# Kernel tuning notes

Measured on AMD Instinct MI355X. Metric: run time of the kernel, lower is better.

## Reference

```python
import jax, jax.numpy as jnp
import numpy as np

N_NODES = 100000
N_EDGES = 1600000
D_FEAT = 64
EPS = 1e-07


def setup_inputs() -> dict:
    key = jax.random.key(0)
    k1, k2, k3 = jax.random.split(key, 3)
    x = jax.random.normal(k1, (N_NODES, D_FEAT), dtype=jnp.float32)
    beta = jnp.ones((1,), dtype=jnp.float32)
    edge_row = jnp.sort(jax.random.randint(k2, (N_EDGES,), 0, N_NODES, dtype=jnp.int64))
    edge_col = jax.random.randint(k3, (N_EDGES,), 0, N_NODES, dtype=jnp.int64)
    return {"x": x, "beta": beta, "edge_row": edge_row, "edge_col": edge_col}


def reference(x, beta, edge_row, edge_col):
    # Gather endpoint features: [E, d]
    A = x[edge_row]
    B = x[edge_col]
    # Cosine similarity per edge, scaled by beta: [E]
    inner = jnp.sum(A * B, axis=1)
    norms = jnp.linalg.norm(A, axis=1) * jnp.linalg.norm(B, axis=1)
    sim = beta[0] * (inner / (norms + EPS))
    # Sparse row-wise softmax (tf.sparse.softmax): stable segment softmax over edges grouped by row
    row_max = jax.ops.segment_max(sim, edge_row, num_segments=N_NODES)
    e = jnp.exp(sim - row_max[edge_row])
    row_sum = jax.ops.segment_sum(e, edge_row, num_segments=N_NODES)
    p = e / row_sum[edge_row]  # [E]
    # SPMM: out[i] = sum_{(i,j) in E} p_ij * x[j]
    out = jax.ops.segment_sum(p[:, None] * B, edge_row, num_segments=N_NODES)
    return out
```

## Files before the change

### kernel.cpp

```cpp
#include <hip/hip_runtime.h>
#include <math.h>

#define D_FEAT 64

__global__ __launch_bounds__(256)
void agnn_rnorm(const float* __restrict__ x, float* __restrict__ rn, int n_nodes) {
    int t = blockIdx.x * blockDim.x + threadIdx.x;
    int node = t >> 4;
    if (node >= n_nodes) return;
    int l4 = t & 15;
    float4 v = ((const float4*)x)[node * 16 + l4];
    float ss = v.x * v.x + v.y * v.y + v.z * v.z + v.w * v.w;
    #pragma unroll
    for (int off = 1; off < 16; off <<= 1)
        ss += __shfl_xor(ss, off, 64);
    if (l4 == 0) rn[node] = ss > 0.f ? rsqrtf(ss) : 0.f;
}

__global__ __launch_bounds__(256)
void agnn_rowptr(const int* __restrict__ edge_row, int* __restrict__ row_ptr,
                 int n_nodes, int n_edges) {
    int e = blockIdx.x * blockDim.x + threadIdx.x;
    if (e >= n_edges) return;
    int r1 = edge_row[e];
    int r0 = (e == 0) ? -1 : edge_row[e - 1];
    for (int r = r0 + 1; r <= r1; ++r) row_ptr[r] = e;
    if (e == n_edges - 1) {
        for (int r = r1 + 1; r <= n_nodes; ++r) row_ptr[r] = n_edges;
    }
}

__global__ __launch_bounds__(256)
void agnn_fused(const float* __restrict__ x,
                const float* __restrict__ beta_p,
                const int* __restrict__ edge_col,
                const int* __restrict__ row_ptr,
                const float* __restrict__ rn,
                float* __restrict__ out, int n_nodes) {
    int node = (blockIdx.x * blockDim.x + threadIdx.x) >> 6;
    if (node >= n_nodes) return;
    int lane = threadIdx.x & 63;
    int g  = lane >> 4;
    int l4 = lane & 15;

    const float4* x4 = (const float4*)x;
    float4 xi  = x4[node * 16 + l4];
    float beta = beta_p[0];
    float brni = beta * rn[node];
    float shift = fabsf(beta);

    int es = row_ptr[node];
    int deg = row_ptr[node + 1] - es;

    float s = 0.f;
    float4 acc = {0.f, 0.f, 0.f, 0.f};

    for (int base = 0; base < deg; base += 8) {
        int ei0 = base + g;
        int ei1 = base + 4 + g;
        bool v0 = ei0 < deg;
        bool v1 = ei1 < deg;
        int ea = es + (v0 ? ei0 : 0);
        int eb = es + (v1 ? ei1 : 0);
        int c0 = edge_col[ea];
        int c1 = edge_col[eb];
        float4 a = x4[c0 * 16 + l4];
        float4 b = x4[c1 * 16 + l4];
        float rn0 = rn[c0];
        float rn1 = rn[c1];

        float d0 = a.x * xi.x + a.y * xi.y + a.z * xi.z + a.w * xi.w;
        float d1 = b.x * xi.x + b.y * xi.y + b.z * xi.z + b.w * xi.w;
        #pragma unroll
        for (int off = 1; off < 16; off <<= 1) {
            d0 += __shfl_xor(d0, off, 64);
            d1 += __shfl_xor(d1, off, 64);
        }

        float w0 = v0 ? __expf(brni * d0 * rn0 - shift) : 0.f;
        float w1 = v1 ? __expf(brni * d1 * rn1 - shift) : 0.f;
        s += w0 + w1;
        acc.x += w0 * a.x + w1 * b.x;
        acc.y += w0 * a.y + w1 * b.y;
        acc.z += w0 * a.z + w1 * b.z;
        acc.w += w0 * a.w + w1 * b.w;
    }

    #pragma unroll
    for (int off = 16; off < 64; off <<= 1) {
        s     += __shfl_xor(s,     off, 64);
        acc.x += __shfl_xor(acc.x, off, 64);
        acc.y += __shfl_xor(acc.y, off, 64);
        acc.z += __shfl_xor(acc.z, off, 64);
        acc.w += __shfl_xor(acc.w, off, 64);
    }

    if (g == 0) {
        float inv = (deg > 0 && s > 0.f) ? 1.f / s : 0.f;
        float4 o = {acc.x * inv, acc.y * inv, acc.z * inv, acc.w * inv};
        ((float4*)out)[node * 16 + l4] = o;
    }
}

extern "C" void kernel_launch(void* const* d_in, const int* in_sizes, int n_in,
                              void* d_out, int out_size, void* d_ws, size_t ws_size,
                              hipStream_t stream) {
    const float* x        = (const float*)d_in[0];
    const float* beta     = (const float*)d_in[1];
    const int*   edge_row = (const int*)d_in[2];
    const int*   edge_col = (const int*)d_in[3];
    float* out = (float*)d_out;

    int n_nodes = in_sizes[0] / D_FEAT;
    int n_edges = in_sizes[2];

    float* rn = (float*)d_ws;
    size_t rn_bytes = ((size_t)n_nodes * sizeof(float) + 255) & ~(size_t)255;
    int* row_ptr = (int*)((char*)d_ws + rn_bytes);

    {
        long long threads = (long long)n_nodes * 16;
        int blocks = (int)((threads + 255) / 256);
        agnn_rnorm<<<blocks, 256, 0, stream>>>(x, rn, n_nodes);
    }
    {
        int blocks = (n_edges + 255) / 256;
        agnn_rowptr<<<blocks, 256, 0, stream>>>(edge_row, row_ptr, n_nodes, n_edges);
    }
    {
        int blocks = (n_nodes + 3) / 4;
        agnn_fused<<<blocks, 256, 0, stream>>>(x, beta, edge_col, row_ptr, rn,
                                               out, n_nodes);
    }
}
```

Measured before the change: 150.3 us.

## Gather neighbor features from a bf16 copy with 8-lane edge groups

```diff
diff --git a/kernel.cpp b/kernel.cpp
--- a/kernel.cpp
+++ b/kernel.cpp
@@ -2,9 +2,17 @@
 #include <math.h>
 
 #define D_FEAT 64
+typedef unsigned int u32;
+
+__device__ __forceinline__ unsigned short f2bf_rne(float f) {
+    u32 u = __float_as_uint(f);
+    u32 r = u + 0x7FFFu + ((u >> 16) & 1u);
+    return (unsigned short)(r >> 16);
+}
 
 __global__ __launch_bounds__(256)
-void agnn_rnorm(const float* __restrict__ x, float* __restrict__ rn, int n_nodes) {
+void agnn_prep(const float* __restrict__ x, float* __restrict__ rn,
+               ushort4* __restrict__ xh, int n_nodes) {
     int t = blockIdx.x * blockDim.x + threadIdx.x;
     int node = t >> 4;
     if (node >= n_nodes) return;
@@ -15,6 +23,10 @@
     for (int off = 1; off < 16; off <<= 1)
         ss += __shfl_xor(ss, off, 64);
     if (l4 == 0) rn[node] = ss > 0.f ? rsqrtf(ss) : 0.f;
+    ushort4 h;
+    h.x = f2bf_rne(v.x); h.y = f2bf_rne(v.y);
+    h.z = f2bf_rne(v.z); h.w = f2bf_rne(v.w);
+    xh[node * 16 + l4] = h;
 }
 
 __global__ __launch_bounds__(256)
@@ -36,69 +48,82 @@
                 const int* __restrict__ edge_col,
                 const int* __restrict__ row_ptr,
                 const float* __restrict__ rn,
+                const ushort4* __restrict__ xh,
                 float* __restrict__ out, int n_nodes) {
     int node = (blockIdx.x * blockDim.x + threadIdx.x) >> 6;
     if (node >= n_nodes) return;
     int lane = threadIdx.x & 63;
-    int g  = lane >> 4;
-    int l4 = lane & 15;
+    int g  = lane >> 3;
+    int l8 = lane & 7;
 
     const float4* x4 = (const float4*)x;
-    float4 xi  = x4[node * 16 + l4];
+    float4 xiLo = x4[node * 16 + 2 * l8];
+    float4 xiHi = x4[node * 16 + 2 * l8 + 1];
     float beta = beta_p[0];
     float brni = beta * rn[node];
     float shift = fabsf(beta);
 
-    int es = row_ptr[node];
+    int es  = row_ptr[node];
     int deg = row_ptr[node + 1] - es;
 
     float s = 0.f;
-    float4 acc = {0.f, 0.f, 0.f, 0.f};
+    float4 accLo = {0.f, 0.f, 0.f, 0.f};
+    float4 accHi = {0.f, 0.f, 0.f, 0.f};
+
+    const uint4* xh4 = (const uint4*)xh;
 
     for (int base = 0; base < deg; base += 8) {
-        int ei0 = base + g;
-        int ei1 = base + 4 + g;
-        bool v0 = ei0 < deg;
-        bool v1 = ei1 < deg;
-        int ea = es + (v0 ? ei0 : 0);
-        int eb = es + (v1 ? ei1 : 0);
-        int c0 = edge_col[ea];
-        int c1 = edge_col[eb];
-        float4 a = x4[c0 * 16 + l4];
-        float4 b = x4[c1 * 16 + l4];
-        float rn0 = rn[c0];
-        float rn1 = rn[c1];
-
-        float d0 = a.x * xi.x + a.y * xi.y + a.z * xi.z + a.w * xi.w;
-        float d1 = b.x * xi.x + b.y * xi.y + b.z * xi.z + b.w * xi.w;
+        int ei = base + g;
+        bool valid = ei < deg;
+        float4 aLo = {0.f, 0.f, 0.f, 0.f};
+        float4 aHi = {0.f, 0.f, 0.f, 0.f};
+        float rnc = 0.f;
+        if (valid) {
+            int c = edge_col[es + ei];
+            uint4 u = xh4[(size_t)c * 8 + l8];
+            rnc = rn[c];
+            aLo.x = __uint_as_float(u.x << 16);
+            aLo.y = __uint_as_float(u.x & 0xFFFF0000u);
+            aLo.z = __uint_as_float(u.y << 16);
+            aLo.w = __uint_as_float(u.y & 0xFFFF0000u);
+            aHi.x = __uint_as_float(u.z << 16);
+            aHi.y = __uint_as_float(u.z & 0xFFFF0000u);
+            aHi.z = __uint_as_float(u.w << 16);
+            aHi.w = __uint_as_float(u.w & 0xFFFF0000u);
+        }
+        float d = aLo.x * xiLo.x + aLo.y * xiLo.y + aLo.z * xiLo.z + aLo.w * xiLo.w
+                + aHi.x * xiHi.x + aHi.y * xiHi.y + aHi.z * xiHi.z + aHi.w * xiHi.w;
         #pragma unroll
-        for (int off = 1; off < 16; off <<= 1) {
-            d0 += __shfl_xor(d0, off, 64);
-            d1 += __shfl_xor(d1, off, 64);
-        }
-
-        float w0 = v0 ? __expf(brni * d0 * rn0 - shift) : 0.f;
-        float w1 = v1 ? __expf(brni * d1 * rn1 - shift) : 0.f;
-        s += w0 + w1;
-        acc.x += w0 * a.x + w1 * b.x;
-        acc.y += w0 * a.y + w1 * b.y;
-        acc.z += w0 * a.z + w1 * b.z;
-        acc.w += w0 * a.w + w1 * b.w;
+        for (int off = 1; off < 8; off <<= 1)
+            d += __shfl_xor(d, off, 64);
+        float w = valid ? __expf(brni * d * rnc - shift) : 0.f;
+        s += w;
+        accLo.x += w * aLo.x; accLo.y += w * aLo.y;
+        accLo.z += w * aLo.z; accLo.w += w * aLo.w;
+        accHi.x += w * aHi.x; accHi.y += w * aHi.y;
+        accHi.z += w * aHi.z; accHi.w += w * aHi.w;
     }
 
     #pragma unroll
-    for (int off = 16; off < 64; off <<= 1) {
-        s     += __shfl_xor(s,     off, 64);
-        acc.x += __shfl_xor(acc.x, off, 64);
-        acc.y += __shfl_xor(acc.y, off, 64);
-        acc.z += __shfl_xor(acc.z, off, 64);
-        acc.w += __shfl_xor(acc.w, off, 64);
+    for (int off = 8; off < 64; off <<= 1) {
+        s       += __shfl_xor(s,       off, 64);
+        accLo.x += __shfl_xor(accLo.x, off, 64);
+        accLo.y += __shfl_xor(accLo.y, off, 64);
+        accLo.z += __shfl_xor(accLo.z, off, 64);
+        accLo.w += __shfl_xor(accLo.w, off, 64);
+        accHi.x += __shfl_xor(accHi.x, off, 64);
+        accHi.y += __shfl_xor(accHi.y, off, 64);
+        accHi.z += __shfl_xor(accHi.z, off, 64);
+        accHi.w += __shfl_xor(accHi.w, off, 64);
     }
 
     if (g == 0) {
         float inv = (deg > 0 && s > 0.f) ? 1.f / s : 0.f;
-        float4 o = {acc.x * inv, acc.y * inv, acc.z * inv, acc.w * inv};
-        ((float4*)out)[node * 16 + l4] = o;
+        float4 oLo = {accLo.x * inv, accLo.y * inv, accLo.z * inv, accLo.w * inv};
+        float4 oHi = {accHi.x * inv, accHi.y * inv, accHi.z * inv, accHi.w * inv};
+        float4* o4 = (float4*)out;
+        o4[node * 16 + 2 * l8]     = oLo;
+        o4[node * 16 + 2 * l8 + 1] = oHi;
     }
 }
 
@@ -114,14 +139,17 @@
     int n_nodes = in_sizes[0] / D_FEAT;
     int n_edges = in_sizes[2];
 
-    float* rn = (float*)d_ws;
-    size_t rn_bytes = ((size_t)n_nodes * sizeof(float) + 255) & ~(size_t)255;
-    int* row_ptr = (int*)((char*)d_ws + rn_bytes);
+    char* ws = (char*)d_ws;
+    float* rn = (float*)ws;
+    size_t off0 = ((size_t)n_nodes * sizeof(float) + 255) & ~(size_t)255;
+    int* row_ptr = (int*)(ws + off0);
+    size_t off1 = off0 + (((size_t)(n_nodes + 1) * sizeof(int) + 255) & ~(size_t)255);
+    ushort4* xh = (ushort4*)(ws + off1);
 
     {
         long long threads = (long long)n_nodes * 16;
         int blocks = (int)((threads + 255) / 256);
-        agnn_rnorm<<<blocks, 256, 0, stream>>>(x, rn, n_nodes);
+        agnn_prep<<<blocks, 256, 0, stream>>>(x, rn, xh, n_nodes);
     }
     {
         int blocks = (n_edges + 255) / 256;
@@ -130,6 +158,6 @@
     {
         int blocks = (n_nodes + 3) / 4;
         agnn_fused<<<blocks, 256, 0, stream>>>(x, beta, edge_col, row_ptr, rn,
-                                               out, n_nodes);
+                                               xh, out, n_nodes);
     }
 }
```

Result: faster. 144.5 us (-3.9%).

## Gather neighbor features in fp16 with dot2 and merge prep kernels

Applied to the files above, without the earlier changes.

```diff
diff --git a/kernel.cpp b/kernel.cpp
--- a/kernel.cpp
+++ b/kernel.cpp
@@ -2,31 +2,52 @@
 #include <math.h>
 
 #define D_FEAT 64
+typedef _Float16 h2 __attribute__((ext_vector_type(2)));
 
-__global__ __launch_bounds__(256)
-void agnn_rnorm(const float* __restrict__ x, float* __restrict__ rn, int n_nodes) {
-    int t = blockIdx.x * blockDim.x + threadIdx.x;
-    int node = t >> 4;
-    if (node >= n_nodes) return;
-    int l4 = t & 15;
-    float4 v = ((const float4*)x)[node * 16 + l4];
-    float ss = v.x * v.x + v.y * v.y + v.z * v.z + v.w * v.w;
-    #pragma unroll
-    for (int off = 1; off < 16; off <<= 1)
-        ss += __shfl_xor(ss, off, 64);
-    if (l4 == 0) rn[node] = ss > 0.f ? rsqrtf(ss) : 0.f;
+__device__ __forceinline__ float dot2(unsigned int a, h2 b, float c) {
+    h2 av; __builtin_memcpy(&av, &a, 4);
+#if __has_builtin(__builtin_amdgcn_fdot2)
+    return __builtin_amdgcn_fdot2(av, b, c, false);
+#else
+    return c + (float)av[0] * (float)b[0] + (float)av[1] * (float)b[1];
+#endif
+}
+
+__device__ __forceinline__ h2 bits2h2(unsigned int a) {
+    h2 av; __builtin_memcpy(&av, &a, 4);
+    return av;
 }
 
 __global__ __launch_bounds__(256)
-void agnn_rowptr(const int* __restrict__ edge_row, int* __restrict__ row_ptr,
-                 int n_nodes, int n_edges) {
-    int e = blockIdx.x * blockDim.x + threadIdx.x;
-    if (e >= n_edges) return;
-    int r1 = edge_row[e];
-    int r0 = (e == 0) ? -1 : edge_row[e - 1];
-    for (int r = r0 + 1; r <= r1; ++r) row_ptr[r] = e;
-    if (e == n_edges - 1) {
-        for (int r = r1 + 1; r <= n_nodes; ++r) row_ptr[r] = n_edges;
+void agnn_prep(const float* __restrict__ x, float* __restrict__ rn,
+               uint2* __restrict__ xh, const int* __restrict__ edge_row,
+               int* __restrict__ row_ptr, int n_nodes, int n_edges, int nb_prep) {
+    if ((int)blockIdx.x < nb_prep) {
+        int t = blockIdx.x * blockDim.x + threadIdx.x;
+        int node = t >> 4;
+        if (node >= n_nodes) return;
+        int l4 = t & 15;
+        float4 v = ((const float4*)x)[node * 16 + l4];
+        float ss = v.x * v.x + v.y * v.y + v.z * v.z + v.w * v.w;
+        #pragma unroll
+        for (int off = 1; off < 16; off <<= 1)
+            ss += __shfl_xor(ss, off, 64);
+        if (l4 == 0) rn[node] = ss > 0.f ? rsqrtf(ss) : 0.f;
+        h2 h0 = {( _Float16)v.x, (_Float16)v.y};
+        h2 h1 = {( _Float16)v.z, (_Float16)v.w};
+        uint2 u;
+        __builtin_memcpy(&u.x, &h0, 4);
+        __builtin_memcpy(&u.y, &h1, 4);
+        xh[node * 16 + l4] = u;
+    } else {
+        int e = (blockIdx.x - nb_prep) * blockDim.x + threadIdx.x;
+        if (e >= n_edges) return;
+        int r1 = edge_row[e];
+        int r0 = (e == 0) ? -1 : edge_row[e - 1];
+        for (int r = r0 + 1; r <= r1; ++r) row_ptr[r] = e;
+        if (e == n_edges - 1) {
+            for (int r = r1 + 1; r <= n_nodes; ++r) row_ptr[r] = n_edges;
+        }
     }
 }
 
@@ -36,43 +57,61 @@
                 const int* __restrict__ edge_col,
                 const int* __restrict__ row_ptr,
                 const float* __restrict__ rn,
+                const uint4* __restrict__ xh4,
                 float* __restrict__ out, int n_nodes) {
     int node = (blockIdx.x * blockDim.x + threadIdx.x) >> 6;
     if (node >= n_nodes) return;
     int lane = threadIdx.x & 63;
-    int g  = lane >> 4;
-    int l4 = lane & 15;
+    int g  = lane >> 3;
+    int l8 = lane & 7;
 
     const float4* x4 = (const float4*)x;
-    float4 xi  = x4[node * 16 + l4];
+    float4 xiLo = x4[node * 16 + 2 * l8];
+    float4 xiHi = x4[node * 16 + 2 * l8 + 1];
+    h2 xi0 = {( _Float16)xiLo.x, (_Float16)xiLo.y};
+    h2 xi1 = {( _Float16)xiLo.z, (_Float16)xiLo.w};
+    h2 xi2 = {( _Float16)xiHi.x, (_Float16)xiHi.y};
+    h2 xi3 = {( _Float16)xiHi.z, (_Float16)xiHi.w};
+
     float beta = beta_p[0];
     float brni = beta * rn[node];
     float shift = fabsf(beta);
 
-    int es = row_ptr[node];
+    int es  = row_ptr[node];
     int deg = row_ptr[node + 1] - es;
 
     float s = 0.f;
-    float4 acc = {0.f, 0.f, 0.f, 0.f};
+    h2 acc0 = {0, 0}, acc1 = {0, 0}, acc2 = {0, 0}, acc3 = {0, 0};
 
-    for (int base = 0; base < deg; base += 8) {
+    for (int base = 0; base < deg; base += 16) {
         int ei0 = base + g;
-        int ei1 = base + 4 + g;
+        int ei1 = base + 8 + g;
         bool v0 = ei0 < deg;
         bool v1 = ei1 < deg;
-        int ea = es + (v0 ? ei0 : 0);
-        int eb = es + (v1 ? ei1 : 0);
-        int c0 = edge_col[ea];
-        int c1 = edge_col[eb];
-        float4 a = x4[c0 * 16 + l4];
-        float4 b = x4[c1 * 16 + l4];
-        float rn0 = rn[c0];
-        float rn1 = rn[c1];
+        uint4 u0 = {0, 0, 0, 0};
+        uint4 u1 = {0, 0, 0, 0};
+        float rn0 = 0.f, rn1 = 0.f;
+        if (v0) {
+            int c = edge_col[es + ei0];
+            u0 = xh4[(size_t)c * 8 + l8];
+            rn0 = rn[c];
+        }
+        if (v1) {
+            int c = edge_col[es + ei1];
+            u1 = xh4[(size_t)c * 8 + l8];
+            rn1 = rn[c];
+        }
 
-        float d0 = a.x * xi.x + a.y * xi.y + a.z * xi.z + a.w * xi.w;
-        float d1 = b.x * xi.x + b.y * xi.y + b.z * xi.z + b.w * xi.w;
+        float d0 = dot2(u0.x, xi0, 0.f);
+        d0 = dot2(u0.y, xi1, d0);
+        d0 = dot2(u0.z, xi2, d0);
+        d0 = dot2(u0.w, xi3, d0);
+        float d1 = dot2(u1.x, xi0, 0.f);
+        d1 = dot2(u1.y, xi1, d1);
+        d1 = dot2(u1.z, xi2, d1);
+        d1 = dot2(u1.w, xi3, d1);
         #pragma unroll
-        for (int off = 1; off < 16; off <<= 1) {
+        for (int off = 1; off < 8; off <<= 1) {
             d0 += __shfl_xor(d0, off, 64);
             d1 += __shfl_xor(d1, off, 64);
         }
@@ -80,25 +119,43 @@
         float w0 = v0 ? __expf(brni * d0 * rn0 - shift) : 0.f;
         float w1 = v1 ? __expf(brni * d1 * rn1 - shift) : 0.f;
         s += w0 + w1;
-        acc.x += w0 * a.x + w1 * b.x;
-        acc.y += w0 * a.y + w1 * b.y;
-        acc.z += w0 * a.z + w1 * b.z;
-        acc.w += w0 * a.w + w1 * b.w;
+
+        h2 w02 = {( _Float16)w0, (_Float16)w0};
+        h2 w12 = {( _Float16)w1, (_Float16)w1};
+        acc0 = bits2h2(u0.x) * w02 + acc0;
+        acc1 = bits2h2(u0.y) * w02 + acc1;
+        acc2 = bits2h2(u0.z) * w02 + acc2;
+        acc3 = bits2h2(u0.w) * w02 + acc3;
+        acc0 = bits2h2(u1.x) * w12 + acc0;
+        acc1 = bits2h2(u1.y) * w12 + acc1;
+        acc2 = bits2h2(u1.z) * w12 + acc2;
+        acc3 = bits2h2(u1.w) * w12 + acc3;
     }
 
+    float f0 = (float)acc0[0], f1 = (float)acc0[1];
+    float f2 = (float)acc1[0], f3 = (float)acc1[1];
+    float f4 = (float)acc2[0], f5 = (float)acc2[1];
+    float f6 = (float)acc3[0], f7 = (float)acc3[1];
     #pragma unroll
-    for (int off = 16; off < 64; off <<= 1) {
-        s     += __shfl_xor(s,     off, 64);
-        acc.x += __shfl_xor(acc.x, off, 64);
-        acc.y += __shfl_xor(acc.y, off, 64);
-        acc.z += __shfl_xor(acc.z, off, 64);
-        acc.w += __shfl_xor(acc.w, off, 64);
+    for (int off = 8; off < 64; off <<= 1) {
+        s  += __shfl_xor(s,  off, 64);
+        f0 += __shfl_xor(f0, off, 64);
+        f1 += __shfl_xor(f1, off, 64);
+        f2 += __shfl_xor(f2, off, 64);
+        f3 += __shfl_xor(f3, off, 64);
+        f4 += __shfl_xor(f4, off, 64);
+        f5 += __shfl_xor(f5, off, 64);
+        f6 += __shfl_xor(f6, off, 64);
+        f7 += __shfl_xor(f7, off, 64);
     }
 
     if (g == 0) {
         float inv = (deg > 0 && s > 0.f) ? 1.f / s : 0.f;
-        float4 o = {acc.x * inv, acc.y * inv, acc.z * inv, acc.w * inv};
-        ((float4*)out)[node * 16 + l4] = o;
+        float4 oLo = {f0 * inv, f1 * inv, f2 * inv, f3 * inv};
+        float4 oHi = {f4 * inv, f5 * inv, f6 * inv, f7 * inv};
+        float4* o4 = (float4*)out;
+        o4[node * 16 + 2 * l8]     = oLo;
+        o4[node * 16 + 2 * l8 + 1] = oHi;
     }
 }
 
@@ -114,22 +171,22 @@
     int n_nodes = in_sizes[0] / D_FEAT;
     int n_edges = in_sizes[2];
 
-    float* rn = (float*)d_ws;
-    size_t rn_bytes = ((size_t)n_nodes * sizeof(float) + 255) & ~(size_t)255;
-    int* row_ptr = (int*)((char*)d_ws + rn_bytes);
+    char* ws = (char*)d_ws;
+    float* rn = (float*)ws;
+    size_t off0 = ((size_t)n_nodes * sizeof(float) + 255) & ~(size_t)255;
+    int* row_ptr = (int*)(ws + off0);
+    size_t off1 = off0 + (((size_t)(n_nodes + 1) * sizeof(int) + 255) & ~(size_t)255);
+    uint2* xh = (uint2*)(ws + off1);
 
     {
-        long long threads = (long long)n_nodes * 16;
-        int blocks = (int)((threads + 255) / 256);
-        agnn_rnorm<<<blocks, 256, 0, stream>>>(x, rn, n_nodes);
-    }
-    {
-        int blocks = (n_edges + 255) / 256;
-        agnn_rowptr<<<blocks, 256, 0, stream>>>(edge_row, row_ptr, n_nodes, n_edges);
+        int nb_prep = (n_nodes * 16 + 255) / 256;
+        int nb_rp   = (n_edges + 255) / 256;
+        agnn_prep<<<nb_prep + nb_rp, 256, 0, stream>>>(
+            x, rn, xh, edge_row, row_ptr, n_nodes, n_edges, nb_prep);
     }
     {
         int blocks = (n_nodes + 3) / 4;
         agnn_fused<<<blocks, 256, 0, stream>>>(x, beta, edge_col, row_ptr, rn,
-                                               out, n_nodes);
+                                               (const uint4*)xh, out, n_nodes);
     }
 }
```

After: 137.3 us. 8.7% less time.
